# Optimization experiments

Measured on AMD Instinct MI355X. Metric: run time of the kernel, lower is better.

The kernel has to match this reference:

```python
import jax, jax.numpy as jnp
import numpy as np
from jax import lax

K = 3
STRIDE = 1
PAD = 1


def _active_sites(mask):
    # mask: [B, Cm, H, W] int. A patch is 'active' if ANY element of the
    # unfolded (im2col) patch is nonzero -> max-pool of (mask != 0) over the
    # same kernel/stride/padding window.
    m = jnp.any(mask != 0, axis=1, keepdims=True).astype(jnp.float32)  # [B,1,H,W]
    pooled = lax.reduce_window(
        m, 0.0, lax.max,
        window_dimensions=(1, 1, K, K),
        window_strides=(1, 1, STRIDE, STRIDE),
        padding=((0, 0), (0, 0), (PAD, PAD), (PAD, PAD)))
    return pooled > 0  # [B,1,H_out,W_out] bool


def reference(x, mask, weight, bias):
    # Faithful math of MyConv: conv2d(x, weight) + bias at active patch sites
    # (patches whose mask window contains any nonzero), exact zeros elsewhere.
    # masked_scatter in the original preserves patch order, so this equals
    # active * (conv + bias).
    conv = lax.conv_general_dilated(
        x, weight,
        window_strides=(STRIDE, STRIDE),
        padding=((PAD, PAD), (PAD, PAD)),
        dimension_numbers=('NCHW', 'OIHW', 'NCHW'))  # [B,C_out,H_out,W_out]
    active = _active_sites(mask)
    out = (conv + bias[None, :, None, None]) * active.astype(conv.dtype)
    return out


def setup_inputs() -> dict:
    key = jax.random.key(0)
    k1, k2, k3, k4 = jax.random.split(key, 4)
    B, C_in, C_out, H, W = 8, 128, 128, 128, 128
    x = jax.random.normal(k1, (B, C_in, H, W), dtype=jnp.float32)
    mask = jax.random.randint(k2, (B, 1, H, W), 0, 2, dtype=jnp.int32)
    fan_in = C_in * K * K
    bound = 1.0 / np.sqrt(fan_in)
    weight = jax.random.uniform(k3, (C_out, C_in, K, K), minval=-bound, maxval=bound, dtype=jnp.float32)
    bias = jax.random.uniform(k4, (C_out,), minval=-bound, maxval=bound, dtype=jnp.float32)
    return {"x": x, "mask": mask, "weight": weight, "bias": bias}
```

## Files before the change

kernel.cpp:

```cpp
#include <hip/hip_runtime.h>


typedef __bf16 bf16x8 __attribute__((ext_vector_type(8)));
typedef unsigned short u16x8 __attribute__((ext_vector_type(8)));
typedef float f32x4 __attribute__((ext_vector_type(4)));

__device__ __forceinline__ unsigned short f2bf(float f) {
    unsigned int u = __float_as_uint(f);
    u += 0x7fffu + ((u >> 16) & 1u);
    return (unsigned short)(u >> 16);
}

__global__ void setup_wp(const float* __restrict__ wgt, unsigned short* __restrict__ wpp) {
    const int e    = blockIdx.x * 256 + threadIdx.x;
    const int j    = e & 31;
    const int m    = (e >> 5) & 127;
    const int r    = e >> 12;
    const int kw   = r - (r / 3) * 3;
    const int cbkh = r / 3;
    const int cb   = cbkh & 3;
    const int kh   = cbkh >> 2;
    const int ci   = 4 * (j & 7) + (j >> 3);
    wpp[e] = f2bf(wgt[((m * 128 + cb * 32 + ci) * 3 + kh) * 3 + kw]);
}

__device__ __forceinline__ void stage1(const float* __restrict__ x,
                                       unsigned char* slab,
                                       int b, int cb, int h, int t) {
    const int rr   = (t & 127) + 1;
    const int cswz = (rr + (rr >> 2)) & 3;
    const int lc0  = (t >> 7) << 1;
    const bool inb = (unsigned)h < 128u;
    const float* xr = x + ((((b * 128 + cb * 32) * 128) + h) << 7) + (rr - 1);
    #pragma unroll
    for (int d = 0; d < 2; ++d) {
        const int lc = lc0 + d;
        u16x8 o = {0, 0, 0, 0, 0, 0, 0, 0};
        if (inb) {
            #pragma unroll
            for (int s = 0; s < 8; ++s)
                o[s] = f2bf(xr[(lc << 14) + (s << 16)]);
        }
        *(u16x8*)(slab + rr * 64 + ((lc ^ cswz) << 4)) = o;
    }
}

__global__ __launch_bounds__(256, 2)
void myconv12(const float* __restrict__ x,
              const int* __restrict__ mask,
              const unsigned short* __restrict__ wp,
              const float* __restrict__ bias,
              float* __restrict__ out)
{
    __shared__ __align__(16) unsigned char Xs[4 * 8320];
    __shared__ float act[256];

    const int t = threadIdx.x;
    const int b  = blockIdx.x & 7;
    const int h0 = (blockIdx.x >> 3) << 1;

    const int lane  = t & 63;
    const int l16   = lane & 15;
    const int q     = lane >> 4;
    const int g     = (t >> 6) & 1;
    const int mhalf = t >> 7;

    if (t < 32) {
        const u16x8 z = {0, 0, 0, 0, 0, 0, 0, 0};
        const int p  = t >> 3;
        const int rr = (t & 4) ? 129 : 0;
        const int c  = t & 3;
        *(u16x8*)(&Xs[p * 8320] + rr * 64 + (c << 4)) = z;
    }

    {
        const int gg = t >> 7;
        const int w  = t & 127;
        const int h  = h0 + gg;
        int any = 0;
        #pragma unroll
        for (int kh = 0; kh < 3; ++kh) {
            int hh = h + kh - 1;
            if ((unsigned)hh < 128u) {
                const int* mrow = mask + (b * 128 + hh) * 128;
                #pragma unroll
                for (int kw = 0; kw < 3; ++kw) {
                    int ww = w + kw - 1;
                    if ((unsigned)ww < 128u) any |= mrow[ww];
                }
            }
        }
        act[t] = any ? 1.0f : 0.0f;
    }

    #pragma unroll
    for (int y = 0; y < 4; ++y)
        stage1(x, &Xs[y * 8320], b, 0, h0 - 1 + y, t);

    int bb[3];
    #pragma unroll
    for (int kw = 0; kw < 3; ++kw) {
        const int rr   = l16 + kw;
        const int slot = q ^ ((rr + (rr >> 2)) & 3);
        bb[kw] = rr * 64 + (slot << 4);
    }

    const unsigned char* agl = (const unsigned char*)wp + (mhalf * 64 + l16) * 64 + q * 16;

    f32x4 acc[4][8];
    const f32x4 fzero = {0.f, 0.f, 0.f, 0.f};
    #pragma unroll
    for (int i = 0; i < 4; ++i)
        #pragma unroll
        for (int j = 0; j < 8; ++j)
            acc[i][j] = fzero;

    __syncthreads();

#define COMPUTE_KH(k)                                                          \
    {                                                                          \
        const unsigned char* ar = agl + ((k) * 4 + cb) * 24576;                \
        const unsigned char* xb = &Xs[((k) + g) * 8320];                       \
        _Pragma("unroll")                                                      \
        for (int kw = 0; kw < 3; ++kw) {                                       \
            bf16x8 af[4];                                                      \
            _Pragma("unroll")                                                  \
            for (int i = 0; i < 4; ++i)                                        \
                af[i] = *(const bf16x8*)(ar + kw * 8192 + i * 1024);           \
            bf16x8 bfr[8];                                                     \
            _Pragma("unroll")                                                  \
            for (int j = 0; j < 8; ++j)                                        \
                bfr[j] = *(const bf16x8*)(xb + bb[kw] + j * 1024);             \
            _Pragma("unroll")                                                  \
            for (int i = 0; i < 4; ++i)                                        \
                _Pragma("unroll")                                              \
                for (int j = 0; j < 8; ++j)                                    \
                    acc[i][j] = __builtin_amdgcn_mfma_f32_16x16x32_bf16(       \
                        af[i], bfr[j], acc[i][j], 0, 0, 0);                    \
        }                                                                      \
    }

    for (int cb = 0; cb < 4; ++cb) {
        if (cb > 0) {
            stage1(x, &Xs[2 * 8320], b, cb, h0 + 1, t);
            stage1(x, &Xs[3 * 8320], b, cb, h0 + 2, t);
        }
        COMPUTE_KH(0);
        __syncthreads();

        if (cb < 3) stage1(x, &Xs[0 * 8320], b, cb + 1, h0 - 1, t);
        COMPUTE_KH(1);
        __syncthreads();

        if (cb < 3) stage1(x, &Xs[1 * 8320], b, cb + 1, h0 + 0, t);
        COMPUTE_KH(2);
        __syncthreads();
    }
#undef COMPUTE_KH

    #pragma unroll
    for (int i = 0; i < 4; ++i) {
        const int m0 = mhalf * 64 + (i << 4) + (q << 2);
        const f32x4 bv = *(const f32x4*)(bias + m0);
        #pragma unroll
        for (int j = 0; j < 8; ++j) {
            const int w = (j << 4) + l16;
            const float a = act[(g << 7) + w];
            float* base = out + (((b << 7) + m0) << 14) + ((h0 + g) << 7) + w;
            #pragma unroll
            for (int rg = 0; rg < 4; ++rg)
                base[rg << 14] = (acc[i][j][rg] + bv[rg]) * a;
        }
    }
}

#define LDAF 40
__global__ __launch_bounds__(256, 2)
void myconv_fb(const float* __restrict__ x,
               const int* __restrict__ mask,
               const float* __restrict__ wgt,
               const float* __restrict__ bias,
               float* __restrict__ out)
{
    __shared__ unsigned short As[128 * LDAF];
    __shared__ unsigned short Bs[128 * LDAF];
    __shared__ float act[128];

    const int t   = threadIdx.x;
    const int blk = blockIdx.x;
    const int b   = blk >> 7;
    const int h   = blk & 127;

    if (t < 128) {
        int any = 0;
        #pragma unroll
        for (int kh = 0; kh < 3; ++kh) {
            int hh = h + kh - 1;
            if ((unsigned)hh < 128u) {
                const int* mrow = mask + (b * 128 + hh) * 128;
                #pragma unroll
                for (int kw = 0; kw < 3; ++kw) {
                    int ww = t + kw - 1;
                    if ((unsigned)ww < 128u) any |= mrow[ww];
                }
            }
        }
        act[t] = any ? 1.0f : 0.0f;
    }

    const int lane = t & 63;
    const int l16  = lane & 15;
    const int half = lane >> 4;
    const int wv   = t >> 6;
    const int wm   = (wv >> 1) << 6;
    const int wn   = (wv & 1) << 6;

    f32x4 acc[4][4];
    const f32x4 fzero = {0.f, 0.f, 0.f, 0.f};
    #pragma unroll
    for (int i = 0; i < 4; ++i)
        #pragma unroll
        for (int j = 0; j < 4; ++j)
            acc[i][j] = fzero;

    const int am  = t >> 3;
    const int ac4 = (t & 7) << 2;
    const int n     = t & 127;
    const int khalf = __builtin_amdgcn_readfirstlane(t >> 7);
    const int xb    = b << 21;

    for (int kt = 0; kt < 36; ++kt) {
        __syncthreads();
        #pragma unroll
        for (int jj = 0; jj < 4; ++jj) {
            const int m = am + (jj << 5);
            const float4 v = *(const float4*)(wgt + m * 1152 + kt * 32 + ac4);
            unsigned short* dst = &As[m * LDAF + ac4];
            dst[0] = f2bf(v.x); dst[1] = f2bf(v.y); dst[2] = f2bf(v.z); dst[3] = f2bf(v.w);
        }
        u16x8 bv0, bv1;
        #pragma unroll
        for (int s = 0; s < 16; ++s) {
            const int k  = kt * 32 + khalf * 16 + s;
            const int ci = (k * 7282) >> 16;
            const int r  = k - ci * 9;
            const int kh = (r >= 3) + (r >= 6);
            const int kw = r - kh * 3;
            const int hh = h + kh - 1;
            float v = 0.f;
            if ((unsigned)hh < 128u) {
                const int ww = n + kw - 1;
                if ((unsigned)ww < 128u)
                    v = x[xb + (ci << 14) + (hh << 7) + ww];
            }
            if (s < 8) bv0[s] = f2bf(v); else bv1[s - 8] = f2bf(v);
        }
        *(u16x8*)&Bs[n * LDAF + khalf * 16]     = bv0;
        *(u16x8*)&Bs[n * LDAF + khalf * 16 + 8] = bv1;

        __syncthreads();

        bf16x8 af[4], bfr[4];
        #pragma unroll
        for (int i = 0; i < 4; ++i)
            af[i] = *(const bf16x8*)&As[(wm + (i << 4) + l16) * LDAF + (half << 3)];
        #pragma unroll
        for (int j = 0; j < 4; ++j)
            bfr[j] = *(const bf16x8*)&Bs[(wn + (j << 4) + l16) * LDAF + (half << 3)];
        #pragma unroll
        for (int i = 0; i < 4; ++i)
            #pragma unroll
            for (int j = 0; j < 4; ++j)
                acc[i][j] = __builtin_amdgcn_mfma_f32_16x16x32_bf16(af[i], bfr[j], acc[i][j], 0, 0, 0);
    }

    #pragma unroll
    for (int i = 0; i < 4; ++i) {
        #pragma unroll
        for (int j = 0; j < 4; ++j) {
            const int ncol = wn + (j << 4) + l16;
            const float a  = act[ncol];
            #pragma unroll
            for (int rg = 0; rg < 4; ++rg) {
                const int m = wm + (i << 4) + (half << 2) + rg;
                out[(((b << 7) + m) << 14) + (h << 7) + ncol] =
                    (acc[i][j][rg] + bias[m]) * a;
            }
        }
    }
}

extern "C" void kernel_launch(void* const* d_in, const int* in_sizes, int n_in,
                              void* d_out, int out_size, void* d_ws, size_t ws_size,
                              hipStream_t stream) {
    const float* x    = (const float*)d_in[0];
    const int*   mask = (const int*)d_in[1];
    const float* wgt  = (const float*)d_in[2];
    const float* bias = (const float*)d_in[3];
    float* out        = (float*)d_out;

    const size_t WP_ELEMS = 36ull * 128 * 32;
    if (ws_size >= WP_ELEMS * 2) {
        unsigned short* wpw = (unsigned short*)d_ws;
        setup_wp<<<dim3(576), dim3(256), 0, stream>>>(wgt, wpw);
        myconv12<<<dim3(512), dim3(256), 0, stream>>>(x, mask, wpw, bias, out);
    } else {
        myconv_fb<<<dim3(1024), dim3(256), 0, stream>>>(x, mask, wgt, bias, out);
    }
}
```

Baseline: 139.9 us.

## Split conv tile along width to halve accumulators and raise occupancy

Each block now covers 64 output columns instead of 128, so the grid doubles to 1024 blocks. The per-thread accumulator array shrinks from 4x8 to 4x4 MFMA tiles, shared slabs shrink to 66 columns with halo, and launch bounds ask for 4 blocks per CU. The aim is more waves in flight to hide the global loads and fp32-to-bf16 conversion. The cost is more weight-fragment reloads per output and extra halo loads at block edges.

```diff
diff --git a/kernel.cpp b/kernel.cpp
--- a/kernel.cpp
+++ b/kernel.cpp
@@ -24,40 +24,48 @@
     wpp[e] = f2bf(wgt[((m * 128 + cb * 32 + ci) * 3 + kh) * 3 + kw]);
 }
 
+#define SLAB 4224
+
+__device__ __forceinline__ void stage_slot(const float* __restrict__ x,
+                                           unsigned char* slab,
+                                           int b, int cb, int h, int w0,
+                                           int p, int lc) {
+    const int gw    = w0 - 1 + p;
+    const bool val  = ((unsigned)h < 128u) & ((unsigned)gw < 128u);
+    u16x8 o = {0, 0, 0, 0, 0, 0, 0, 0};
+    if (val) {
+        const float* xr = x + ((((b * 128 + cb * 32) * 128) + h) << 7) + gw;
+        #pragma unroll
+        for (int s = 0; s < 8; ++s)
+            o[s] = f2bf(xr[(lc << 14) + (s << 16)]);
+    }
+    *(u16x8*)(slab + p * 64 + ((lc ^ ((p + (p >> 2)) & 3)) << 4)) = o;
+}
+
 __device__ __forceinline__ void stage1(const float* __restrict__ x,
                                        unsigned char* slab,
-                                       int b, int cb, int h, int t) {
-    const int rr   = (t & 127) + 1;
-    const int cswz = (rr + (rr >> 2)) & 3;
-    const int lc0  = (t >> 7) << 1;
-    const bool inb = (unsigned)h < 128u;
-    const float* xr = x + ((((b * 128 + cb * 32) * 128) + h) << 7) + (rr - 1);
-    #pragma unroll
-    for (int d = 0; d < 2; ++d) {
-        const int lc = lc0 + d;
-        u16x8 o = {0, 0, 0, 0, 0, 0, 0, 0};
-        if (inb) {
-            #pragma unroll
-            for (int s = 0; s < 8; ++s)
-                o[s] = f2bf(xr[(lc << 14) + (s << 16)]);
-        }
-        *(u16x8*)(slab + rr * 64 + ((lc ^ cswz) << 4)) = o;
-    }
-}
-
-__global__ __launch_bounds__(256, 2)
-void myconv12(const float* __restrict__ x,
+                                       int b, int cb, int h, int w0, int t) {
+    const int lc = t >> 6;
+    const int p  = t & 63;
+    stage_slot(x, slab, b, cb, h, w0, p, lc);
+    if (p < 2) stage_slot(x, slab, b, cb, h, w0, p + 64, lc);
+}
+
+__global__ __launch_bounds__(256, 4)
+void myconv13(const float* __restrict__ x,
               const int* __restrict__ mask,
               const unsigned short* __restrict__ wp,
               const float* __restrict__ bias,
               float* __restrict__ out)
 {
-    __shared__ __align__(16) unsigned char Xs[4 * 8320];
-    __shared__ float act[256];
+    __shared__ __align__(16) unsigned char Xs[4 * SLAB];
+    __shared__ float act[128];
 
     const int t = threadIdx.x;
-    const int b  = blockIdx.x & 7;
-    const int h0 = (blockIdx.x >> 3) << 1;
+    const int b     = blockIdx.x & 7;
+    const int whalf = (blockIdx.x >> 3) & 1;
+    const int h0    = ((blockIdx.x >> 4) & 63) << 1;
+    const int w0    = whalf << 6;
 
     const int lane  = t & 63;
     const int l16   = lane & 15;
@@ -65,17 +73,9 @@
     const int g     = (t >> 6) & 1;
     const int mhalf = t >> 7;
 
-    if (t < 32) {
-        const u16x8 z = {0, 0, 0, 0, 0, 0, 0, 0};
-        const int p  = t >> 3;
-        const int rr = (t & 4) ? 129 : 0;
-        const int c  = t & 3;
-        *(u16x8*)(&Xs[p * 8320] + rr * 64 + (c << 4)) = z;
-    }
-
-    {
-        const int gg = t >> 7;
-        const int w  = t & 127;
+    if (t < 128) {
+        const int gg = t >> 6;
+        const int wl = t & 63;
         const int h  = h0 + gg;
         int any = 0;
         #pragma unroll
@@ -85,7 +85,7 @@
                 const int* mrow = mask + (b * 128 + hh) * 128;
                 #pragma unroll
                 for (int kw = 0; kw < 3; ++kw) {
-                    int ww = w + kw - 1;
+                    int ww = w0 + wl + kw - 1;
                     if ((unsigned)ww < 128u) any |= mrow[ww];
                 }
             }
@@ -95,7 +95,7 @@
 
     #pragma unroll
     for (int y = 0; y < 4; ++y)
-        stage1(x, &Xs[y * 8320], b, 0, h0 - 1 + y, t);
+        stage1(x, &Xs[y * SLAB], b, 0, h0 - 1 + y, w0, t);
 
     int bb[3];
     #pragma unroll
@@ -107,12 +107,12 @@
 
     const unsigned char* agl = (const unsigned char*)wp + (mhalf * 64 + l16) * 64 + q * 16;
 
-    f32x4 acc[4][8];
+    f32x4 acc[4][4];
     const f32x4 fzero = {0.f, 0.f, 0.f, 0.f};
     #pragma unroll
     for (int i = 0; i < 4; ++i)
         #pragma unroll
-        for (int j = 0; j < 8; ++j)
+        for (int j = 0; j < 4; ++j)
             acc[i][j] = fzero;
 
     __syncthreads();
@@ -120,21 +120,21 @@
 #define COMPUTE_KH(k)                                                          \
     {                                                                          \
         const unsigned char* ar = agl + ((k) * 4 + cb) * 24576;                \
-        const unsigned char* xb = &Xs[((k) + g) * 8320];                       \
+        const unsigned char* xb = &Xs[((k) + g) * SLAB];                       \
         _Pragma("unroll")                                                      \
         for (int kw = 0; kw < 3; ++kw) {                                       \
             bf16x8 af[4];                                                      \
             _Pragma("unroll")                                                  \
             for (int i = 0; i < 4; ++i)                                        \
                 af[i] = *(const bf16x8*)(ar + kw * 8192 + i * 1024);           \
-            bf16x8 bfr[8];                                                     \
+            bf16x8 bfr[4];                                                     \
             _Pragma("unroll")                                                  \
-            for (int j = 0; j < 8; ++j)                                        \
+            for (int j = 0; j < 4; ++j)                                        \
                 bfr[j] = *(const bf16x8*)(xb + bb[kw] + j * 1024);             \
             _Pragma("unroll")                                                  \
             for (int i = 0; i < 4; ++i)                                        \
                 _Pragma("unroll")                                              \
-                for (int j = 0; j < 8; ++j)                                    \
+                for (int j = 0; j < 4; ++j)                                    \
                     acc[i][j] = __builtin_amdgcn_mfma_f32_16x16x32_bf16(       \
                         af[i], bfr[j], acc[i][j], 0, 0, 0);                    \
         }                                                                      \
@@ -142,17 +142,17 @@
 
     for (int cb = 0; cb < 4; ++cb) {
         if (cb > 0) {
-            stage1(x, &Xs[2 * 8320], b, cb, h0 + 1, t);
-            stage1(x, &Xs[3 * 8320], b, cb, h0 + 2, t);
+            stage1(x, &Xs[2 * SLAB], b, cb, h0 + 1, w0, t);
+            stage1(x, &Xs[3 * SLAB], b, cb, h0 + 2, w0, t);
         }
         COMPUTE_KH(0);
         __syncthreads();
 
-        if (cb < 3) stage1(x, &Xs[0 * 8320], b, cb + 1, h0 - 1, t);
+        if (cb < 3) stage1(x, &Xs[0 * SLAB], b, cb + 1, h0 - 1, w0, t);
         COMPUTE_KH(1);
         __syncthreads();
 
-        if (cb < 3) stage1(x, &Xs[1 * 8320], b, cb + 1, h0 + 0, t);
+        if (cb < 3) stage1(x, &Xs[1 * SLAB], b, cb + 1, h0 + 0, w0, t);
         COMPUTE_KH(2);
         __syncthreads();
     }
@@ -163,10 +163,10 @@
         const int m0 = mhalf * 64 + (i << 4) + (q << 2);
         const f32x4 bv = *(const f32x4*)(bias + m0);
         #pragma unroll
-        for (int j = 0; j < 8; ++j) {
-            const int w = (j << 4) + l16;
-            const float a = act[(g << 7) + w];
-            float* base = out + (((b << 7) + m0) << 14) + ((h0 + g) << 7) + w;
+        for (int j = 0; j < 4; ++j) {
+            const int wl = (j << 4) + l16;
+            const float a = act[(g << 6) + wl];
+            float* base = out + (((b << 7) + m0) << 14) + ((h0 + g) << 7) + w0 + wl;
             #pragma unroll
             for (int rg = 0; rg < 4; ++rg)
                 base[rg << 14] = (acc[i][j][rg] + bv[rg]) * a;
@@ -303,7 +303,7 @@
     if (ws_size >= WP_ELEMS * 2) {
         unsigned short* wpw = (unsigned short*)d_ws;
         setup_wp<<<dim3(576), dim3(256), 0, stream>>>(wgt, wpw);
-        myconv12<<<dim3(512), dim3(256), 0, stream>>>(x, mask, wpw, bias, out);
+        myconv13<<<dim3(1024), dim3(256), 0, stream>>>(x, mask, wpw, bias, out);
     } else {
         myconv_fb<<<dim3(1024), dim3(256), 0, stream>>>(x, mask, wgt, bias, out);
     }
```

After: 161.6 us. 1.15x slower.
